# Kernel optimization log

Measured on AMD Instinct MI355X. Metric: run time of the kernel, lower is better.

The kernel has to match this reference:

```python
import jax, jax.numpy as jnp
import numpy as np

BATCH = 16384
NNZ = 524288
INPUT_DIM = 30000
OUTPUT_DIM = 300


def setup_inputs() -> dict:
    key = jax.random.key(0)
    k1, k2, k3, k4 = jax.random.split(key, 4)
    sp_rows = jnp.sort(jax.random.randint(k1, (NNZ,), 0, BATCH, dtype=jnp.int32))
    sp_cols = jax.random.randint(k2, (NNZ,), 0, INPUT_DIM, dtype=jnp.int32)
    sp_vals = jax.random.uniform(k3, (NNZ,), dtype=jnp.float32)
    # glorot init for weights, zeros bias (as in the TF module)
    scale = jnp.sqrt(6.0 / (INPUT_DIM + OUTPUT_DIM)).astype(jnp.float32)
    weights = jax.random.uniform(k4, (INPUT_DIM, OUTPUT_DIM), dtype=jnp.float32,
                                 minval=-scale, maxval=scale)
    bias = jnp.zeros((OUTPUT_DIM,), dtype=jnp.float32)
    return {"sp_rows": sp_rows, "sp_cols": sp_cols, "sp_vals": sp_vals,
            "weights": weights, "bias": bias, "batch_size": BATCH}


def reference(sp_rows, sp_cols, sp_vals, weights, bias, batch_size):
    # sparse [batch, input_dim] @ dense [input_dim, output_dim]:
    # gather weight rows per nnz, scale by value, segment-sum into output rows.
    contrib = sp_vals[:, None] * weights[sp_cols]          # [nnz, output_dim]
    dense_vector = jax.ops.segment_sum(contrib, sp_rows,
                                       num_segments=batch_size)  # [batch, output_dim]
    dense_vector = dense_vector + bias
    return jax.nn.relu(dense_vector)
```

## Files before the change

### kernel.cpp

```cpp
#include <hip/hip_runtime.h>

#define OUT_DIM 300
#define SLICES  5
#define SLICE_B 128

typedef _Float16 half8_t __attribute__((ext_vector_type(8)));
typedef unsigned int uint32x4_t __attribute__((ext_vector_type(4)));

__global__ __launch_bounds__(256) void setup5_kernel(
    const int* __restrict__ rows, int* __restrict__ row_ptr,
    const float* __restrict__ w, unsigned char* __restrict__ wf,
    int nnz, int batch, int in_dim, int scat_blocks)
{
    if ((int)blockIdx.x < scat_blocks) {
        int i = blockIdx.x * 256 + threadIdx.x;
        if (i >= nnz) return;
        int r = rows[i];
        int prev = (i == 0) ? -1 : rows[i - 1];
        for (int q = prev + 1; q <= r; ++q) row_ptr[q] = i;
        if (i == nnz - 1)
            for (int q = r + 1; q <= batch; ++q) row_ptr[q] = nnz;
        return;
    }
    int j = ((int)blockIdx.x - scat_blocks) * 256 + threadIdx.x;
    if (j >= in_dim * (SLICES * 8)) return;
    int r   = j / 40;
    int c16 = j - r * 40;
    int s   = c16 >> 3;
    int kc  = c16 & 7;
    int c0  = c16 * 8;
    const float* wr = w + (size_t)r * OUT_DIM + c0;
    float4 f0 = make_float4(0.f, 0.f, 0.f, 0.f);
    float4 f1 = make_float4(0.f, 0.f, 0.f, 0.f);
    if (c0 + 4 <= OUT_DIM) f0 = *(const float4*)wr;
    if (c0 + 8 <= OUT_DIM) f1 = *(const float4*)(wr + 4);
    half8_t h;
    h[0] = (_Float16)f0.x; h[1] = (_Float16)f0.y;
    h[2] = (_Float16)f0.z; h[3] = (_Float16)f0.w;
    h[4] = (_Float16)f1.x; h[5] = (_Float16)f1.y;
    h[6] = (_Float16)f1.z; h[7] = (_Float16)f1.w;
    *(half8_t*)(wf + ((size_t)s * in_dim + r) * SLICE_B + kc * 16) = h;
}

__global__ __launch_bounds__(256, 8) void spmm5p(
    const int* __restrict__ row_ptr,
    const int* __restrict__ cols,
    const float* __restrict__ vals,
    const unsigned char* __restrict__ wf,
    const float* __restrict__ bias,
    float* __restrict__ out,
    int batch, int in_dim, int rowgroups)
{
    __shared__ uint2 sh[4][64];

    const int items = SLICES * rowgroups;
    const int q8  = items >> 3, rm = items & 7;
    const int xcd = (int)blockIdx.x & 7;
    const int bi  = (int)blockIdx.x >> 3;
    const int bpx = (int)gridDim.x >> 3;
    const int it_lo = (xcd < rm) ? xcd * (q8 + 1)
                                 : rm * (q8 + 1) + (xcd - rm) * q8;
    const int it_hi = it_lo + ((xcd < rm) ? (q8 + 1) : q8);

    const int wave  = threadIdx.x >> 6;
    const int lane  = threadIdx.x & 63;
    const int grp   = lane >> 3;
    const int choff = (lane & 7) * 16;
    uint2* shw = sh[wave];

    int it = it_lo + bi;
    if (it >= it_hi) return;

    int slice = it / rowgroups;
    int rg    = it - slice * rowgroups;
    int row   = rg * 4 + wave;
    int lo = 0, hi = 0;
    if (row < batch) { lo = row_ptr[row]; hi = row_ptr[row + 1]; }
    uint2 ov;
    {
        int cnt = hi - lo; if (cnt > 64) cnt = 64;
        if (lane < cnt) {
            ov.x = (unsigned)cols[lo + lane] * SLICE_B;
            ov.y = __float_as_uint(vals[lo + lane]);
        } else { ov.x = 0x40000000u; ov.y = 0u; }
    }

#define FMA8(M, VB)                                            \
    do {                                                       \
        float v_ = __uint_as_float(VB);                        \
        half8_t wv_ = __builtin_bit_cast(half8_t, (M));        \
        a0 += v_ * (float)wv_[0]; a1 += v_ * (float)wv_[1];    \
        a2 += v_ * (float)wv_[2]; a3 += v_ * (float)wv_[3];    \
        a4 += v_ * (float)wv_[4]; a5 += v_ * (float)wv_[5];    \
        a6 += v_ * (float)wv_[6]; a7 += v_ * (float)wv_[7];    \
    } while (0)

#define PROCESS(CNT)                                                          \
    do {                                                                      \
        uint2 q0 = shw[grp], q1 = shw[grp + 8];                               \
        uint2 q2 = shw[grp + 16], q3 = shw[grp + 24];                         \
        uint32x4_t m0 = __builtin_amdgcn_raw_buffer_load_b128(                \
            rsrc, (int)(q0.x + choff), 0, 1);                                 \
        uint32x4_t m1 = __builtin_amdgcn_raw_buffer_load_b128(                \
            rsrc, (int)(q1.x + choff), 0, 1);                                 \
        uint32x4_t m2 = __builtin_amdgcn_raw_buffer_load_b128(                \
            rsrc, (int)(q2.x + choff), 0, 1);                                 \
        uint32x4_t m3 = __builtin_amdgcn_raw_buffer_load_b128(                \
            rsrc, (int)(q3.x + choff), 0, 1);                                 \
        FMA8(m0, q0.y); FMA8(m1, q1.y); FMA8(m2, q2.y); FMA8(m3, q3.y);       \
        if ((CNT) > 32) {                                                     \
            uint2 q4 = shw[grp + 32], q5 = shw[grp + 40];                     \
            uint2 q6 = shw[grp + 48], q7 = shw[grp + 56];                     \
            uint32x4_t m4 = __builtin_amdgcn_raw_buffer_load_b128(            \
                rsrc, (int)(q4.x + choff), 0, 1);                             \
            uint32x4_t m5 = __builtin_amdgcn_raw_buffer_load_b128(            \
                rsrc, (int)(q5.x + choff), 0, 1);                             \
            uint32x4_t m6 = __builtin_amdgcn_raw_buffer_load_b128(            \
                rsrc, (int)(q6.x + choff), 0, 1);                             \
            uint32x4_t m7 = __builtin_amdgcn_raw_buffer_load_b128(            \
                rsrc, (int)(q7.x + choff), 0, 1);                             \
            FMA8(m4, q4.y); FMA8(m5, q5.y); FMA8(m6, q6.y); FMA8(m7, q7.y);   \
        }                                                                     \
    } while (0)

    while (true) {
        const int  it_next    = it + bpx;
        const bool have_next  = it_next < it_hi;

        const unsigned char* wslice = wf + (size_t)slice * in_dim * SLICE_B;
        __amdgpu_buffer_rsrc_t rsrc = __builtin_amdgcn_make_buffer_rsrc(
            (void*)wslice, (short)0, in_dim * SLICE_B, 0x00020000);

        int nslice = 0, nrg = 0, nrow = 0, nlo = 0, nhi = 0;
        if (have_next) {
            nslice = it_next / rowgroups;
            nrg    = it_next - nslice * rowgroups;
            nrow   = nrg * 4 + wave;
            if (nrow < batch) { nlo = row_ptr[nrow]; nhi = row_ptr[nrow + 1]; }
        }

        float a0 = 0.f, a1 = 0.f, a2 = 0.f, a3 = 0.f;
        float a4 = 0.f, a5 = 0.f, a6 = 0.f, a7 = 0.f;

        int cnt0 = hi - lo; if (cnt0 > 64) cnt0 = 64;
        shw[lane] = ov;
        PROCESS(cnt0);

        for (int base = lo + 64; base < hi; base += 64) {
            int c2 = hi - base; if (c2 > 64) c2 = 64;
            uint2 o2;
            if (lane < c2) {
                o2.x = (unsigned)cols[base + lane] * SLICE_B;
                o2.y = __float_as_uint(vals[base + lane]);
            } else { o2.x = 0x40000000u; o2.y = 0u; }
            shw[lane] = o2;
            PROCESS(c2);
        }

        uint2 nov; nov.x = 0x40000000u; nov.y = 0u;
        if (have_next) {
            int ncnt = nhi - nlo; if (ncnt > 64) ncnt = 64;
            if (lane < ncnt) {
                nov.x = (unsigned)cols[nlo + lane] * SLICE_B;
                nov.y = __float_as_uint(vals[nlo + lane]);
            }
        }

        a0 += __shfl_down(a0, 32); a1 += __shfl_down(a1, 32);
        a2 += __shfl_down(a2, 32); a3 += __shfl_down(a3, 32);
        a4 += __shfl_down(a4, 32); a5 += __shfl_down(a5, 32);
        a6 += __shfl_down(a6, 32); a7 += __shfl_down(a7, 32);
        a0 += __shfl_down(a0, 16); a1 += __shfl_down(a1, 16);
        a2 += __shfl_down(a2, 16); a3 += __shfl_down(a3, 16);
        a4 += __shfl_down(a4, 16); a5 += __shfl_down(a5, 16);
        a6 += __shfl_down(a6, 16); a7 += __shfl_down(a7, 16);
        a0 += __shfl_down(a0, 8);  a1 += __shfl_down(a1, 8);
        a2 += __shfl_down(a2, 8);  a3 += __shfl_down(a3, 8);
        a4 += __shfl_down(a4, 8);  a5 += __shfl_down(a5, 8);
        a6 += __shfl_down(a6, 8);  a7 += __shfl_down(a7, 8);

        if (lane < 8 && row < batch) {
            const int col = slice * 64 + lane * 8;
            if (col + 4 <= OUT_DIM) {
                float* orow = out + (size_t)row * OUT_DIM + col;
                const float4 b0 = *(const float4*)(bias + col);
                float4 s0;
                s0.x = fmaxf(a0 + b0.x, 0.f);
                s0.y = fmaxf(a1 + b0.y, 0.f);
                s0.z = fmaxf(a2 + b0.z, 0.f);
                s0.w = fmaxf(a3 + b0.w, 0.f);
                *(float4*)orow = s0;
                if (col + 8 <= OUT_DIM) {
                    const float4 b1 = *(const float4*)(bias + col + 4);
                    float4 s1;
                    s1.x = fmaxf(a4 + b1.x, 0.f);
                    s1.y = fmaxf(a5 + b1.y, 0.f);
                    s1.z = fmaxf(a6 + b1.z, 0.f);
                    s1.w = fmaxf(a7 + b1.w, 0.f);
                    *(float4*)(orow + 4) = s1;
                }
            }
        }

        if (!have_next) break;
        it = it_next; slice = nslice; rg = nrg; row = nrow;
        lo = nlo; hi = nhi; ov = nov;
    }
#undef PROCESS
#undef FMA8
}

__global__ __launch_bounds__(256) void row_ptr_scatter(
    const int* __restrict__ rows, int* __restrict__ row_ptr, int nnz, int batch)
{
    int i = blockIdx.x * 256 + threadIdx.x;
    if (i >= nnz) return;
    int r = rows[i];
    int prev = (i == 0) ? -1 : rows[i - 1];
    for (int q = prev + 1; q <= r; ++q) row_ptr[q] = i;
    if (i == nnz - 1)
        for (int q = r + 1; q <= batch; ++q) row_ptr[q] = nnz;
}

__global__ __launch_bounds__(256) void spmm_wave_f32_kernel(
    const int* __restrict__ row_ptr,
    const int* __restrict__ cols,
    const float* __restrict__ vals,
    const float* __restrict__ weights,
    const float* __restrict__ bias,
    float* __restrict__ out,
    int batch)
{
    const int wave = threadIdx.x >> 6;
    const int lane = threadIdx.x & 63;
    const int row  = blockIdx.x * 4 + wave;
    if (row >= batch) return;

    const int lo = row_ptr[row];
    const int hi = row_ptr[row + 1];
    float4 acc0 = make_float4(0.f, 0.f, 0.f, 0.f);
    float4 acc1 = make_float4(0.f, 0.f, 0.f, 0.f);
    const bool tail = (lane < 75 - 64);

    for (int base = lo; base < hi; base += 64) {
        const int rem = hi - base;
        const int cnt = rem < 64 ? rem : 64;
        int   c = 0;
        float v = 0.0f;
        if (lane < cnt) { c = cols[base + lane]; v = vals[base + lane]; }
        const int rounds = (cnt + 7) & ~7;
        for (int k = 0; k < rounds; k += 8) {
#pragma unroll
            for (int u = 0; u < 8; ++u) {
                const int   cc = __shfl(c, k + u);
                const float vv = __shfl(v, k + u);
                const float4* wrow = (const float4*)(weights + (size_t)cc * OUT_DIM);
                float4 w0 = wrow[lane];
                acc0.x += vv * w0.x; acc0.y += vv * w0.y;
                acc0.z += vv * w0.z; acc0.w += vv * w0.w;
                if (tail) {
                    float4 w1 = wrow[64 + lane];
                    acc1.x += vv * w1.x; acc1.y += vv * w1.y;
                    acc1.z += vv * w1.z; acc1.w += vv * w1.w;
                }
            }
        }
    }

    const float4* b4 = (const float4*)bias;
    float4* orow = (float4*)(out + (size_t)row * OUT_DIM);
    float4 b0 = b4[lane];
    float4 r0;
    r0.x = fmaxf(acc0.x + b0.x, 0.f);
    r0.y = fmaxf(acc0.y + b0.y, 0.f);
    r0.z = fmaxf(acc0.z + b0.z, 0.f);
    r0.w = fmaxf(acc0.w + b0.w, 0.f);
    orow[lane] = r0;
    if (tail) {
        float4 b1 = b4[64 + lane];
        float4 r1;
        r1.x = fmaxf(acc1.x + b1.x, 0.f);
        r1.y = fmaxf(acc1.y + b1.y, 0.f);
        r1.z = fmaxf(acc1.z + b1.z, 0.f);
        r1.w = fmaxf(acc1.w + b1.w, 0.f);
        orow[64 + lane] = r1;
    }
}

extern "C" void kernel_launch(void* const* d_in, const int* in_sizes, int n_in,
                              void* d_out, int out_size, void* d_ws, size_t ws_size,
                              hipStream_t stream) {
    const int*   sp_rows = (const int*)d_in[0];
    const int*   sp_cols = (const int*)d_in[1];
    const float* sp_vals = (const float*)d_in[2];
    const float* weights = (const float*)d_in[3];
    const float* bias    = (const float*)d_in[4];
    float* out = (float*)d_out;

    const int nnz    = in_sizes[0];
    const int w_elts = in_sizes[3];
    const int in_dim = w_elts / OUT_DIM;
    const int batch  = out_size / OUT_DIM;

    size_t rp_bytes = (size_t)(batch + 1) * sizeof(int);
    size_t wf_off   = (rp_bytes + 255) & ~(size_t)255;
    size_t need5    = wf_off + (size_t)in_dim * SLICES * SLICE_B + 256;

    int* row_ptr = (int*)d_ws;
    const int rowgroups = (batch + 3) / 4;

    if (ws_size >= need5) {
        unsigned char* wf = (unsigned char*)d_ws + wf_off;
        const int scat_blocks = (nnz + 255) / 256;
        const int rep_blocks  = (in_dim * (SLICES * 8) + 255) / 256;
        setup5_kernel<<<scat_blocks + rep_blocks, 256, 0, stream>>>(
            sp_rows, row_ptr, weights, wf, nnz, batch, in_dim, scat_blocks);
        spmm5p<<<2048, 256, 0, stream>>>(
            row_ptr, sp_cols, sp_vals, wf, bias, out, batch, in_dim, rowgroups);
    } else {
        row_ptr_scatter<<<(nnz + 255) / 256, 256, 0, stream>>>(
            sp_rows, row_ptr, nnz, batch);
        spmm_wave_f32_kernel<<<(batch + 3) / 4, 256, 0, stream>>>(
            row_ptr, sp_cols, sp_vals, weights, bias, out, batch);
    }
}
```

Before: 133.5 us.

## Fuse setup and SpMM into one persistent kernel with grid barrier and prefetch

Merges the row_ptr scatter and fp16 weight repack kernels into the SpMM kernel, using a grid-stride prologue and an atomic global barrier, so there is one launch plus a memset. The SpMM loop is also restructured into a software pipeline: the gather loads for the next pair of 8-entry groups, and for the next work item's first groups, are issued before the current FMAs, with double-buffered shared memory. This targets launch and inter-kernel gap overhead and exposed gather latency. The grid barrier depends on all 1792 blocks being co-resident, so it risks deadlock if occupancy falls short, and the barrier adds spin time.

```diff
diff --git a/kernel.cpp b/kernel.cpp
--- a/kernel.cpp
+++ b/kernel.cpp
@@ -7,51 +7,61 @@
 typedef _Float16 half8_t __attribute__((ext_vector_type(8)));
 typedef unsigned int uint32x4_t __attribute__((ext_vector_type(4)));
 
-__global__ __launch_bounds__(256) void setup5_kernel(
-    const int* __restrict__ rows, int* __restrict__ row_ptr,
-    const float* __restrict__ w, unsigned char* __restrict__ wf,
-    int nnz, int batch, int in_dim, int scat_blocks)
+__global__ __launch_bounds__(256, 8) void fused5(
+    const int* __restrict__ rows,
+    const int* __restrict__ cols,
+    const float* __restrict__ vals,
+    const float* __restrict__ w,
+    const float* __restrict__ bias,
+    float* __restrict__ out,
+    int* __restrict__ row_ptr,
+    unsigned char* __restrict__ wf,
+    unsigned int* __restrict__ bar,
+    int nnz, int batch, int in_dim, int rowgroups)
 {
-    if ((int)blockIdx.x < scat_blocks) {
-        int i = blockIdx.x * 256 + threadIdx.x;
-        if (i >= nnz) return;
+    __shared__ uint2 sh[4][2][64];
+
+    const int nth  = (int)gridDim.x * 256;
+    const int gtid = (int)blockIdx.x * 256 + (int)threadIdx.x;
+
+    const int nchunk = in_dim * (SLICES * 8);
+    for (int j = gtid; j < nchunk; j += nth) {
+        int r   = j / 40;
+        int c16 = j - r * 40;
+        int s   = c16 >> 3;
+        int kc  = c16 & 7;
+        int c0  = c16 * 8;
+        const float* wr = w + (size_t)r * OUT_DIM + c0;
+        float4 f0 = make_float4(0.f, 0.f, 0.f, 0.f);
+        float4 f1 = make_float4(0.f, 0.f, 0.f, 0.f);
+        if (c0 + 4 <= OUT_DIM) f0 = *(const float4*)wr;
+        if (c0 + 8 <= OUT_DIM) f1 = *(const float4*)(wr + 4);
+        half8_t h;
+        h[0] = (_Float16)f0.x; h[1] = (_Float16)f0.y;
+        h[2] = (_Float16)f0.z; h[3] = (_Float16)f0.w;
+        h[4] = (_Float16)f1.x; h[5] = (_Float16)f1.y;
+        h[6] = (_Float16)f1.z; h[7] = (_Float16)f1.w;
+        *(half8_t*)(wf + ((size_t)s * in_dim + r) * SLICE_B + kc * 16) = h;
+    }
+    for (int i = gtid; i < nnz; i += nth) {
         int r = rows[i];
         int prev = (i == 0) ? -1 : rows[i - 1];
         for (int q = prev + 1; q <= r; ++q) row_ptr[q] = i;
         if (i == nnz - 1)
             for (int q = r + 1; q <= batch; ++q) row_ptr[q] = nnz;
-        return;
-    }
-    int j = ((int)blockIdx.x - scat_blocks) * 256 + threadIdx.x;
-    if (j >= in_dim * (SLICES * 8)) return;
-    int r   = j / 40;
-    int c16 = j - r * 40;
-    int s   = c16 >> 3;
-    int kc  = c16 & 7;
-    int c0  = c16 * 8;
-    const float* wr = w + (size_t)r * OUT_DIM + c0;
-    float4 f0 = make_float4(0.f, 0.f, 0.f, 0.f);
-    float4 f1 = make_float4(0.f, 0.f, 0.f, 0.f);
-    if (c0 + 4 <= OUT_DIM) f0 = *(const float4*)wr;
-    if (c0 + 8 <= OUT_DIM) f1 = *(const float4*)(wr + 4);
-    half8_t h;
-    h[0] = (_Float16)f0.x; h[1] = (_Float16)f0.y;
-    h[2] = (_Float16)f0.z; h[3] = (_Float16)f0.w;
-    h[4] = (_Float16)f1.x; h[5] = (_Float16)f1.y;
-    h[6] = (_Float16)f1.z; h[7] = (_Float16)f1.w;
-    *(half8_t*)(wf + ((size_t)s * in_dim + r) * SLICE_B + kc * 16) = h;
-}
-
-__global__ __launch_bounds__(256, 8) void spmm5p(
-    const int* __restrict__ row_ptr,
-    const int* __restrict__ cols,
-    const float* __restrict__ vals,
-    const unsigned char* __restrict__ wf,
-    const float* __restrict__ bias,
-    float* __restrict__ out,
-    int batch, int in_dim, int rowgroups)
-{
-    __shared__ uint2 sh[4][64];
+    }
+
+    __syncthreads();
+    if (threadIdx.x == 0) {
+        __builtin_amdgcn_fence(__ATOMIC_RELEASE, "agent");
+        __hip_atomic_fetch_add(bar, 1u, __ATOMIC_RELAXED,
+                               __HIP_MEMORY_SCOPE_AGENT);
+        while (__hip_atomic_load(bar, __ATOMIC_RELAXED,
+                                 __HIP_MEMORY_SCOPE_AGENT) < (unsigned)gridDim.x)
+            __builtin_amdgcn_s_sleep(4);
+    }
+    __syncthreads();
+    __builtin_amdgcn_fence(__ATOMIC_ACQUIRE, "agent");
 
     const int items = SLICES * rowgroups;
     const int q8  = items >> 3, rm = items & 7;
@@ -66,85 +76,95 @@
     const int lane  = threadIdx.x & 63;
     const int grp   = lane >> 3;
     const int choff = (lane & 7) * 16;
-    uint2* shw = sh[wave];
 
     int it = it_lo + bi;
     if (it >= it_hi) return;
 
     int slice = it / rowgroups;
-    int rg    = it - slice * rowgroups;
-    int row   = rg * 4 + wave;
+    int row   = (it - slice * rowgroups) * 4 + wave;
     int lo = 0, hi = 0;
     if (row < batch) { lo = row_ptr[row]; hi = row_ptr[row + 1]; }
-    uint2 ov;
+
+    int  itn   = it + bpx;
+    bool have1 = itn < it_hi;
+    int nslice = 0, nrow = 0, nlo = 0, nhi = 0;
+    if (have1) {
+        nslice = itn / rowgroups;
+        nrow   = (itn - nslice * rowgroups) * 4 + wave;
+        if (nrow < batch) { nlo = row_ptr[nrow]; nhi = row_ptr[nrow + 1]; }
+    }
+
+    int par = 0;
     {
         int cnt = hi - lo; if (cnt > 64) cnt = 64;
+        uint2 ov;
         if (lane < cnt) {
             ov.x = (unsigned)cols[lo + lane] * SLICE_B;
             ov.y = __float_as_uint(vals[lo + lane]);
         } else { ov.x = 0x40000000u; ov.y = 0u; }
-    }
-
-#define FMA8(M, VB)                                            \
+        sh[wave][0][lane] = ov;
+    }
+
+    __amdgpu_buffer_rsrc_t rsrc = __builtin_amdgcn_make_buffer_rsrc(
+        (void*)(wf + (size_t)slice * in_dim * SLICE_B), (short)0,
+        in_dim * SLICE_B, 0x00020000);
+
+    uint32x4_t m0, m1; float vm0, vm1;
+    {
+        uint2 t0 = sh[wave][0][grp], t1 = sh[wave][0][8 + grp];
+        m0 = __builtin_amdgcn_raw_buffer_load_b128(rsrc, (int)(t0.x + choff), 0, 1);
+        m1 = __builtin_amdgcn_raw_buffer_load_b128(rsrc, (int)(t1.x + choff), 0, 1);
+        vm0 = __uint_as_float(t0.y); vm1 = __uint_as_float(t1.y);
+    }
+
+#define FMA8(M, V)                                             \
     do {                                                       \
-        float v_ = __uint_as_float(VB);                        \
         half8_t wv_ = __builtin_bit_cast(half8_t, (M));        \
-        a0 += v_ * (float)wv_[0]; a1 += v_ * (float)wv_[1];    \
-        a2 += v_ * (float)wv_[2]; a3 += v_ * (float)wv_[3];    \
-        a4 += v_ * (float)wv_[4]; a5 += v_ * (float)wv_[5];    \
-        a6 += v_ * (float)wv_[6]; a7 += v_ * (float)wv_[7];    \
+        a0 += (V) * (float)wv_[0]; a1 += (V) * (float)wv_[1];  \
+        a2 += (V) * (float)wv_[2]; a3 += (V) * (float)wv_[3];  \
+        a4 += (V) * (float)wv_[4]; a5 += (V) * (float)wv_[5];  \
+        a6 += (V) * (float)wv_[6]; a7 += (V) * (float)wv_[7];  \
     } while (0)
 
-#define PROCESS(CNT)                                                          \
-    do {                                                                      \
-        uint2 q0 = shw[grp], q1 = shw[grp + 8];                               \
-        uint2 q2 = shw[grp + 16], q3 = shw[grp + 24];                         \
-        uint32x4_t m0 = __builtin_amdgcn_raw_buffer_load_b128(                \
-            rsrc, (int)(q0.x + choff), 0, 1);                                 \
-        uint32x4_t m1 = __builtin_amdgcn_raw_buffer_load_b128(                \
-            rsrc, (int)(q1.x + choff), 0, 1);                                 \
-        uint32x4_t m2 = __builtin_amdgcn_raw_buffer_load_b128(                \
-            rsrc, (int)(q2.x + choff), 0, 1);                                 \
-        uint32x4_t m3 = __builtin_amdgcn_raw_buffer_load_b128(                \
-            rsrc, (int)(q3.x + choff), 0, 1);                                 \
-        FMA8(m0, q0.y); FMA8(m1, q1.y); FMA8(m2, q2.y); FMA8(m3, q3.y);       \
-        if ((CNT) > 32) {                                                     \
-            uint2 q4 = shw[grp + 32], q5 = shw[grp + 40];                     \
-            uint2 q6 = shw[grp + 48], q7 = shw[grp + 56];                     \
-            uint32x4_t m4 = __builtin_amdgcn_raw_buffer_load_b128(            \
-                rsrc, (int)(q4.x + choff), 0, 1);                             \
-            uint32x4_t m5 = __builtin_amdgcn_raw_buffer_load_b128(            \
-                rsrc, (int)(q5.x + choff), 0, 1);                             \
-            uint32x4_t m6 = __builtin_amdgcn_raw_buffer_load_b128(            \
-                rsrc, (int)(q6.x + choff), 0, 1);                             \
-            uint32x4_t m7 = __builtin_amdgcn_raw_buffer_load_b128(            \
-                rsrc, (int)(q7.x + choff), 0, 1);                             \
-            FMA8(m4, q4.y); FMA8(m5, q5.y); FMA8(m6, q6.y); FMA8(m7, q7.y);   \
-        }                                                                     \
-    } while (0)
-
     while (true) {
-        const int  it_next    = it + bpx;
-        const bool have_next  = it_next < it_hi;
-
-        const unsigned char* wslice = wf + (size_t)slice * in_dim * SLICE_B;
-        __amdgpu_buffer_rsrc_t rsrc = __builtin_amdgcn_make_buffer_rsrc(
-            (void*)wslice, (short)0, in_dim * SLICE_B, 0x00020000);
-
-        int nslice = 0, nrg = 0, nrow = 0, nlo = 0, nhi = 0;
-        if (have_next) {
-            nslice = it_next / rowgroups;
-            nrg    = it_next - nslice * rowgroups;
-            nrow   = nrg * 4 + wave;
-            if (nrow < batch) { nlo = row_ptr[nrow]; nhi = row_ptr[nrow + 1]; }
+        int  it2   = itn + bpx;
+        bool have2 = have1 && (it2 < it_hi);
+        int n2slice = 0, n2row = 0, n2lo = 0, n2hi = 0;
+        if (have2) {
+            n2slice = it2 / rowgroups;
+            n2row   = (it2 - n2slice * rowgroups) * 4 + wave;
+            if (n2row < batch) { n2lo = row_ptr[n2row]; n2hi = row_ptr[n2row + 1]; }
+        }
+        uint2 nov; nov.x = 0x40000000u; nov.y = 0u;
+        if (have1) {
+            int ncnt = nhi - nlo; if (ncnt > 64) ncnt = 64;
+            if (lane < ncnt) {
+                nov.x = (unsigned)cols[nlo + lane] * SLICE_B;
+                nov.y = __float_as_uint(vals[nlo + lane]);
+            }
         }
 
         float a0 = 0.f, a1 = 0.f, a2 = 0.f, a3 = 0.f;
         float a4 = 0.f, a5 = 0.f, a6 = 0.f, a7 = 0.f;
 
-        int cnt0 = hi - lo; if (cnt0 > 64) cnt0 = 64;
-        shw[lane] = ov;
-        PROCESS(cnt0);
+        int cnt = hi - lo; if (cnt > 64) cnt = 64;
+        int rr  = (cnt + 7) >> 3;
+        int rrp = (rr + 1) & ~1; if (rrp < 2) rrp = 2;
+        const uint2* shw = sh[wave][par];
+        for (int b = 0; ; b += 2) {
+            const bool lastb = (b + 2 >= rrp);
+            uint32x4_t n0v = {}, n1v = {}; float vn0 = 0.f, vn1 = 0.f;
+            if (!lastb) {
+                uint2 p0 = shw[8 * (b + 2) + grp];
+                uint2 p1 = shw[8 * (b + 3) + grp];
+                n0v = __builtin_amdgcn_raw_buffer_load_b128(rsrc, (int)(p0.x + choff), 0, 1);
+                n1v = __builtin_amdgcn_raw_buffer_load_b128(rsrc, (int)(p1.x + choff), 0, 1);
+                vn0 = __uint_as_float(p0.y); vn1 = __uint_as_float(p1.y);
+            }
+            FMA8(m0, vm0); FMA8(m1, vm1);
+            if (lastb) break;
+            m0 = n0v; m1 = n1v; vm0 = vn0; vm1 = vn1;
+        }
 
         for (int base = lo + 64; base < hi; base += 64) {
             int c2 = hi - base; if (c2 > 64) c2 = 64;
@@ -153,17 +173,28 @@
                 o2.x = (unsigned)cols[base + lane] * SLICE_B;
                 o2.y = __float_as_uint(vals[base + lane]);
             } else { o2.x = 0x40000000u; o2.y = 0u; }
-            shw[lane] = o2;
-            PROCESS(c2);
-        }
-
-        uint2 nov; nov.x = 0x40000000u; nov.y = 0u;
-        if (have_next) {
-            int ncnt = nhi - nlo; if (ncnt > 64) ncnt = 64;
-            if (lane < ncnt) {
-                nov.x = (unsigned)cols[nlo + lane] * SLICE_B;
-                nov.y = __float_as_uint(vals[nlo + lane]);
-            }
+            sh[wave][par][lane] = o2;
+            int rr2  = (c2 + 7) >> 3;
+            int rrp2 = (rr2 + 1) & ~1; if (rrp2 < 2) rrp2 = 2;
+            for (int b = 0; b < rrp2; b += 2) {
+                uint2 p0 = shw[8 * b + grp], p1 = shw[8 * (b + 1) + grp];
+                uint32x4_t x0 = __builtin_amdgcn_raw_buffer_load_b128(rsrc, (int)(p0.x + choff), 0, 1);
+                uint32x4_t x1 = __builtin_amdgcn_raw_buffer_load_b128(rsrc, (int)(p1.x + choff), 0, 1);
+                FMA8(x0, __uint_as_float(p0.y));
+                FMA8(x1, __uint_as_float(p1.y));
+            }
+        }
+
+        if (have1) {
+            sh[wave][par ^ 1][lane] = nov;
+            rsrc = __builtin_amdgcn_make_buffer_rsrc(
+                (void*)(wf + (size_t)nslice * in_dim * SLICE_B), (short)0,
+                in_dim * SLICE_B, 0x00020000);
+            const uint2* shn = sh[wave][par ^ 1];
+            uint2 t0 = shn[grp], t1 = shn[8 + grp];
+            m0 = __builtin_amdgcn_raw_buffer_load_b128(rsrc, (int)(t0.x + choff), 0, 1);
+            m1 = __builtin_amdgcn_raw_buffer_load_b128(rsrc, (int)(t1.x + choff), 0, 1);
+            vm0 = __uint_as_float(t0.y); vm1 = __uint_as_float(t1.y);
         }
 
         a0 += __shfl_down(a0, 32); a1 += __shfl_down(a1, 32);
@@ -202,11 +233,12 @@
             }
         }
 
-        if (!have_next) break;
-        it = it_next; slice = nslice; rg = nrg; row = nrow;
-        lo = nlo; hi = nhi; ov = nov;
-    }
-#undef PROCESS
+        if (!have1) break;
+        it = itn; slice = nslice; row = nrow; lo = nlo; hi = nhi;
+        itn = it2; have1 = have2;
+        nslice = n2slice; nrow = n2row; nlo = n2lo; nhi = n2hi;
+        par ^= 1;
+    }
 #undef FMA8
 }
 
@@ -304,19 +336,20 @@
 
     size_t rp_bytes = (size_t)(batch + 1) * sizeof(int);
     size_t wf_off   = (rp_bytes + 255) & ~(size_t)255;
-    size_t need5    = wf_off + (size_t)in_dim * SLICES * SLICE_B + 256;
+    size_t wf_size  = (size_t)in_dim * SLICES * SLICE_B;
+    size_t bar_off  = wf_off + wf_size;
+    size_t need     = bar_off + 256;
 
     int* row_ptr = (int*)d_ws;
     const int rowgroups = (batch + 3) / 4;
 
-    if (ws_size >= need5) {
-        unsigned char* wf = (unsigned char*)d_ws + wf_off;
-        const int scat_blocks = (nnz + 255) / 256;
-        const int rep_blocks  = (in_dim * (SLICES * 8) + 255) / 256;
-        setup5_kernel<<<scat_blocks + rep_blocks, 256, 0, stream>>>(
-            sp_rows, row_ptr, weights, wf, nnz, batch, in_dim, scat_blocks);
-        spmm5p<<<2048, 256, 0, stream>>>(
-            row_ptr, sp_cols, sp_vals, wf, bias, out, batch, in_dim, rowgroups);
+    if (ws_size >= need) {
+        unsigned char* wf  = (unsigned char*)d_ws + wf_off;
+        unsigned int*  bar = (unsigned int*)((unsigned char*)d_ws + bar_off);
+        hipMemsetAsync(bar, 0, 4, stream);
+        fused5<<<1792, 256, 0, stream>>>(
+            sp_rows, sp_cols, sp_vals, weights, bias, out,
+            row_ptr, wf, bar, nnz, batch, in_dim, rowgroups);
     } else {
         row_ptr_scatter<<<(nnz + 255) / 256, 256, 0, stream>>>(
             sp_rows, row_ptr, nnz, batch);
```

After: 316.1 us. 2.37x slower.
